# Optimization experiments

Hardware: AMD Instinct MI355X
Metric: run time of the kernel (lower is better)

The kernel has to match this reference:

```python
import jax, jax.numpy as jnp
import numpy as np
import math

D_MODEL = 512
N_HEADS = 8
D_K = 64
BS = 16
SEQ = 512


def setup_inputs() -> dict:
    key = jax.random.key(0)
    ks = jax.random.split(key, 15)
    f = lambda k, sh, s=1.0: jax.random.normal(k, sh, dtype=jnp.float32) * s
    inp = {}
    for i, n in enumerate(["q_mean", "q_cov", "k_mean", "k_cov", "v_mean", "v_cov"]):
        inp[n] = f(ks[i], (BS, SEQ, D_MODEL))
    wscale = 1.0 / math.sqrt(D_MODEL)  # ~xavier
    for i, n in enumerate(["Wq_mean", "Wq_cov", "Wk_mean", "Wk_cov", "Wv_mean", "Wv_cov", "Wo_mean", "Wo_cov"]):
        inp[n] = f(ks[6 + i], (D_MODEL, D_MODEL), wscale)
    inp["gammas"] = f(ks[14], (N_HEADS, 1, 1), 0.5)  # xavier on (h,1,1)
    # causal mask: attend to positions j <= i
    inp["mask"] = jnp.tril(jnp.ones((SEQ, SEQ), dtype=jnp.int32))[None, None]
    return inp


def _heads(x, W):
    # torch Linear: x @ W.T ; bias is 0 by init. -> [bs, h, S, d_k]
    bs = x.shape[0]
    return (x @ W.T).reshape(bs, -1, N_HEADS, D_K).transpose(0, 2, 1, 3)


def _uattention(qm, qc, km, kc, vm, vc, mask, gammas):
    # Wasserstein-2 distance between diagonal Gaussians, fused into matmuls
    mean_d = (-2.0 * jnp.einsum('bhsd,bhtd->bhst', qm, km)
              + jnp.sum(qm ** 2, -1, keepdims=True)
              + jnp.sum(km ** 2, -1, keepdims=True).swapaxes(-1, -2))
    sqc = jnp.sqrt(jnp.clip(qc, 1e-24))
    skc = jnp.sqrt(jnp.clip(kc, 1e-24))
    cov_d = (-2.0 * jnp.einsum('bhsd,bhtd->bhst', sqc, skc)
             + jnp.sum(qc, -1, keepdims=True)
             + jnp.sum(kc, -1, keepdims=True).swapaxes(-1, -2))
    scores = -(mean_d + cov_d) / math.sqrt(D_K)  # [bs,h,S,S]

    maskb = (mask == 0)
    maskf = mask.astype(scores.dtype)

    def _dist(s):
        s_ = jax.nn.softmax(jnp.where(maskb, -1e32, s), axis=-1) * maskf
        cum = jnp.cumsum(s_, axis=-1)
        tot = jnp.sum(s_, axis=-1, keepdims=True)
        idx = jnp.arange(SEQ)
        pos = jnp.abs(idx[None, :] - idx[:, None]).astype(jnp.float32)[None, None]
        return jnp.sqrt(jnp.clip((tot - cum) * pos, 0.0))

    dist_scores = jax.lax.stop_gradient(_dist(scores))  # torch: no_grad + detach
    gamma = -jax.nn.softplus(gammas)[None]  # [1,h,1,1]
    total_effect = jnp.clip(jnp.exp(dist_scores * gamma), 1e-5, 1e5)
    scores = jnp.where(maskb, -1e32, scores * total_effect)
    scores = jax.nn.softmax(scores, axis=-1)
    scores = scores.at[:, :, 0, :].set(0.0)  # zero_pad
    out_mean = jnp.einsum('bhst,bhtd->bhsd', scores, vm)
    out_cov = jnp.einsum('bhst,bhtd->bhsd', scores ** 2, vc)
    return out_mean, out_cov


def reference(q_mean, q_cov, k_mean, k_cov, v_mean, v_cov,
              Wq_mean, Wq_cov, Wk_mean, Wk_cov, Wv_mean, Wv_cov,
              Wo_mean, Wo_cov, gammas, mask):
    bs = q_mean.shape[0]
    qm = _heads(q_mean, Wq_mean)
    qc = _heads(q_cov, Wq_cov)
    km = _heads(k_mean, Wk_mean)
    kc = _heads(k_cov, Wk_cov)
    vm = _heads(v_mean, Wv_mean)
    vc = _heads(v_cov, Wv_cov)
    om, oc = _uattention(qm, qc, km, kc, vm, vc, mask, gammas)
    cm = om.transpose(0, 2, 1, 3).reshape(bs, -1, D_MODEL)
    cc = oc.transpose(0, 2, 1, 3).reshape(bs, -1, D_MODEL)
    return cm @ Wo_mean.T, cc @ Wo_cov.T
```

## Files before the change

### kernel.cpp

```cpp
#include <hip/hip_runtime.h>
#include <hip/hip_bf16.h>

#define SEQ    512
#define DMODEL 512
#define NHEAD  8
#define DK     64
#define BS     16
#define NBH    (BS*NHEAD)
#define HSZ    (SEQ*DK)
#define L2E    1.4426950408889634f

typedef __attribute__((ext_vector_type(8))) short bf16x8;
typedef __attribute__((ext_vector_type(4))) float f32x4;

#define MFMA32(A,B,C) __builtin_amdgcn_mfma_f32_16x16x32_bf16(A,B,C,0,0,0)

#define WS_GAM 16ull
#define WS_AQM 256ull
#define WS_AQC (WS_AQM +  65536ull)
#define WS_BKM (WS_AQM + 131072ull)
#define WS_BKC (WS_AQM + 196608ull)
#define WS_AQF (WS_AQM + 262144ull)
#define WS_BKF (WS_AQM + 327680ull)
#define WS_OM  1048576ull
#define WS_OC  (WS_OM + 4194304ull)
#define WS_BF  (WS_OC + 4194304ull)
#define ARRE   4194304ull
#define A_QMH 0
#define A_QML 1
#define A_SCH 2
#define A_SCL 3
#define A_KMH 4
#define A_SKH 6
#define A_VMT 8
#define A_VCT 9

__device__ __forceinline__ unsigned short* warr(float* wsf, int idx) {
  return (unsigned short*)(wsf + WS_BF) + (size_t)idx * ARRE;
}

__device__ __forceinline__ float bf2f(unsigned short h) {
  union { float f; unsigned u; } v; v.u = ((unsigned)h) << 16; return v.f;
}
__device__ __forceinline__ unsigned short f2bf(float f) {
  union { float f; unsigned u; } v; v.f = f;
  unsigned u = v.u;
  u += 0x7FFFu + ((u >> 16) & 1u);
  return (unsigned short)(u >> 16);
}
__device__ __forceinline__ void ld8_f32(const float* p, float* v) {
  float4 a = *(const float4*)p; float4 b = *(const float4*)(p+4);
  v[0]=a.x;v[1]=a.y;v[2]=a.z;v[3]=a.w;v[4]=b.x;v[5]=b.y;v[6]=b.z;v[7]=b.w;
}
__device__ __forceinline__ unsigned pk2bf(float a, float b) {
  union { float f; unsigned u; } x, y;
  x.f = a; y.f = b;
  return __builtin_amdgcn_perm(y.u + 0x8000u, x.u + 0x8000u, 0x07060302u);
}
__device__ __forceinline__ uint4 cvt8r(const float* t8) {
  uint4 h;
  h.x = pk2bf(t8[0], t8[1]);
  h.y = pk2bf(t8[2], t8[3]);
  h.z = pk2bf(t8[4], t8[5]);
  h.w = pk2bf(t8[6], t8[7]);
  return h;
}
__device__ __forceinline__ uint4 cvt8h(const float* p) {
  float t8[8]; ld8_f32(p, t8); return cvt8r(t8);
}

__global__ void k_gamma(const float* __restrict__ g_in, float* __restrict__ wsf) {
  int t = threadIdx.x;
  if (t >= NHEAD) return;
  float g = g_in[t];
  float sp = (g > 20.f) ? g : log1pf(expf(g));
  float gl = sp * L2E;
  (wsf + WS_GAM)[t] = gl * gl;
}

__global__ __launch_bounds__(256) void k_projM(
    const float* xqm, const float* xqc, const float* xkm, const float* xkc,
    const float* xvm, const float* xvc,
    const float* wqm, const float* wqc, const float* wkm, const float* wkc,
    const float* wvm, const float* wvc,
    float* wsf)
{
  __shared__ __align__(16) unsigned short Ah[4096];
  __shared__ __align__(16) unsigned short Bh[4096];
  const int y = blockIdx.y;
  const float* X; const float* W;
  unsigned short *outh = nullptr, *outl = nullptr;
  float* sums = nullptr;
  float qscale = 1.0f; int mode = 0;
  switch (y) {
    case 0: X=xqm; W=wqm; outh=warr(wsf,A_QMH); outl=warr(wsf,A_QML); sums=wsf+WS_AQM; qscale=0.25f*L2E; mode=0; break;
    case 1: X=xkm; W=wkm; outh=warr(wsf,A_KMH); outl=nullptr;         sums=wsf+WS_BKM; qscale=1.0f;      mode=0; break;
    case 2: X=xqc; W=wqc; outh=warr(wsf,A_SCH); outl=warr(wsf,A_SCL); sums=wsf+WS_AQC; qscale=0.25f*L2E; mode=1; break;
    case 3: X=xkc; W=wkc; outh=warr(wsf,A_SKH); outl=nullptr;         sums=wsf+WS_BKC; qscale=1.0f;      mode=1; break;
    case 4: X=xvm; W=wvm; outh=warr(wsf,A_VMT); mode=2; break;
    default:X=xvc; W=wvc; outh=warr(wsf,A_VCT); mode=2; break;
  }
  const int tid = threadIdx.x;
  const int l = tid & 63, li = l & 15, lg = l >> 4;
  const int w = tid >> 6, wr = w >> 1, wc = w & 1;
  const int blk = blockIdx.x;
  const int xcd = blk & 7, qq = blk >> 3;
  const int m0 = (xcd*8 + (qq & 7)) * 128;
  const int n0 = (qq >> 3) * 128;
  const int r0 = tid >> 2, c0 = tid & 3, r1 = r0 + 64;
  const int wo0 = r0*64 + ((c0 ^ ((r0>>1)&3))*16);
  const int wo1 = r1*64 + ((c0 ^ ((r1>>1)&3))*16);
  int roA[4], roB[4];
#pragma unroll
  for (int mi = 0; mi < 4; ++mi) {
    int r  = wr*64 + mi*16 + li;
    roA[mi] = r*64 + ((lg ^ ((r>>1)&3))*16);
    int rn = wc*64 + mi*16 + li;
    roB[mi] = rn*64 + ((lg ^ ((rn>>1)&3))*16);
  }
  const float* xp0 = X + (size_t)(m0+r0)*DMODEL + c0*8;
  const float* xp1 = X + (size_t)(m0+r1)*DMODEL + c0*8;
  const float* wp0 = W + (size_t)(n0+r0)*DMODEL + c0*8;
  const float* wp1 = W + (size_t)(n0+r1)*DMODEL + c0*8;
  uint4 a0 = cvt8h(xp0);
  uint4 a1 = cvt8h(xp1);
  uint4 b0 = cvt8h(wp0);
  uint4 b1 = cvt8h(wp1);

  f32x4 acc[4][4];
  f32x4 z = {0.f,0.f,0.f,0.f};
#pragma unroll
  for (int a = 0; a < 4; ++a)
#pragma unroll
    for (int b = 0; b < 4; ++b) acc[a][b] = z;

  for (int kt = 0; kt < DMODEL; kt += 32) {
    __syncthreads();
    *(uint4*)((char*)Ah + wo0) = a0;
    *(uint4*)((char*)Ah + wo1) = a1;
    *(uint4*)((char*)Bh + wo0) = b0;
    *(uint4*)((char*)Bh + wo1) = b1;
    __syncthreads();
    if (kt + 32 < DMODEL) {
      a0 = cvt8h(xp0 + kt + 32);
      a1 = cvt8h(xp1 + kt + 32);
      b0 = cvt8h(wp0 + kt + 32);
      b1 = cvt8h(wp1 + kt + 32);
    }
    bf16x8 ah[4], bh[4];
#pragma unroll
    for (int mi = 0; mi < 4; ++mi) {
      ah[mi] = *(const bf16x8*)((const char*)Ah + roA[mi]);
      bh[mi] = *(const bf16x8*)((const char*)Bh + roB[mi]);
    }
#pragma unroll
    for (int mi = 0; mi < 4; ++mi)
#pragma unroll
      for (int nj = 0; nj < 4; ++nj)
        acc[mi][nj] = MFMA32(ah[mi], bh[nj], acc[mi][nj]);
  }

  const int head = ((n0 >> 6) + wc);
  if (mode <= 1) {
    const bool kside = (outl == nullptr);
#pragma unroll
    for (int mi = 0; mi < 4; ++mi)
#pragma unroll
      for (int reg = 0; reg < 4; ++reg) {
        float rs = 0.f;
#pragma unroll
        for (int nj = 0; nj < 4; ++nj) {
          float v = acc[mi][nj][reg];
          if (mode == 0) {
            float vs = (kside) ? bf2f(f2bf(v)) : v;
            rs += vs*vs;
          } else {
            rs += v;
          }
        }
        rs += __shfl_xor(rs, 1); rs += __shfl_xor(rs, 2);
        rs += __shfl_xor(rs, 4); rs += __shfl_xor(rs, 8);
        if (li == 0) {
          int m = m0 + wr*64 + mi*16 + 4*lg + reg;
          sums[((size_t)(m >> 9)*NHEAD + head)*SEQ + (m & 511)] = rs;
        }
      }
#pragma unroll
    for (int mi = 0; mi < 4; ++mi)
#pragma unroll
      for (int nj = 0; nj < 4; ++nj)
#pragma unroll
        for (int reg = 0; reg < 4; ++reg) {
          float v = acc[mi][nj][reg];
          if (mode == 1) v = sqrtf(fmaxf(v, 1e-24f));
          v *= qscale;
          unsigned short h16 = f2bf(v);
          int m = m0 + wr*64 + mi*16 + 4*lg + reg;
          int n = n0 + wc*64 + nj*16 + li;
          size_t dst = ((size_t)((m >> 9)*NHEAD + (n >> 6))*SEQ + (m & 511))*DK + (n & 63);
          outh[dst] = h16;
          if (outl) outl[dst] = f2bf(v - bf2f(h16));
        }
  } else {
#pragma unroll
    for (int mi = 0; mi < 4; ++mi)
#pragma unroll
      for (int nj = 0; nj < 4; ++nj) {
        int mb = m0 + wr*64 + mi*16 + 4*lg;
        int n = n0 + wc*64 + nj*16 + li;
        int b = mb >> 9, s = mb & 511, d = n & 63;
        unsigned e0 = f2bf(acc[mi][nj][0]);
        unsigned e1 = f2bf(acc[mi][nj][1]);
        unsigned e2 = f2bf(acc[mi][nj][2]);
        unsigned e3 = f2bf(acc[mi][nj][3]);
        uint2 pk; pk.x = e0 | (e1 << 16); pk.y = e2 | (e3 << 16);
        *(uint2*)(outh + ((size_t)(b*NHEAD + head)*DK + d)*SEQ + s) = pk;
      }
  }
}

__global__ void k_sumAB(float* wsf) {
  int i = blockIdx.x * 256 + threadIdx.x;
  if (i < NBH*SEQ) {
    (wsf+WS_AQF)[i] = (0.125f*L2E) * ((wsf+WS_AQM)[i] + (wsf+WS_AQC)[i]);
    (wsf+WS_BKF)[i] = (0.125f*L2E) * ((wsf+WS_BKM)[i] + (wsf+WS_BKC)[i]);
  }
}

__global__ __launch_bounds__(128) void k_attn2(float* wsf)
{
  __shared__ float s_bk[SEQ];
  __shared__ float s_tot[2][16];
  __shared__ __align__(16) float s_acc[64][33];

  const unsigned short* qmh = warr(wsf, A_QMH);
  const unsigned short* qml = warr(wsf, A_QML);
  const unsigned short* sch = warr(wsf, A_SCH);
  const unsigned short* scl = warr(wsf, A_SCL);
  const unsigned short* kmh = warr(wsf, A_KMH);
  const unsigned short* skh = warr(wsf, A_SKH);
  const unsigned short* vmT = warr(wsf, A_VMT);
  const unsigned short* vcT = warr(wsf, A_VCT);
  float* omF = wsf + WS_OM;
  float* ocF = wsf + WS_OC;
  const float* AqF = wsf + WS_AQF;
  const float* BkF = wsf + WS_BKF;

  const int tid = threadIdx.x;
  const int l = tid & 63, li = l & 15, lg = l >> 4;
  const int w = tid >> 6;
  const int blk = blockIdx.x;
  const int xcd = blk & 7;
  const int q   = blk >> 3;
  const int bh  = xcd*16 + (q & 15);
  const int rt  = 31 - (q >> 4);
  const int i = rt*16 + li;
  const int ntile = rt + 1;
  const int h0 = (ntile + 1) >> 1;
  const int tstart = w ? h0 : 0;
  const int tend   = w ? ntile : h0;
  const float gam2 = (wsf + WS_GAM)[bh & (NHEAD-1)];
  const float aq = AqF[(size_t)bh*SEQ + i];

  for (int idx = tid; idx < SEQ; idx += 128) s_bk[idx] = BkF[(size_t)bh*SEQ + idx];

  bf16x8 qf[8];
  {
    const unsigned short* qb[4] = {qmh, qml, sch, scl};
#pragma unroll
    for (int part = 0; part < 2; ++part)
#pragma unroll
      for (int hl = 0; hl < 2; ++hl)
#pragma unroll
        for (int ks = 0; ks < 2; ++ks)
          qf[part*4 + ks*2 + hl] =
            *(const bf16x8*)(qb[part*2+hl] + ((size_t)bh*SEQ + i)*DK + ks*32 + lg*8);
  }
  __syncthreads();

  auto score_tile = [&](int t, float* s) {
    const int j0 = t*16;
    f32x4 accA = {0.f,0.f,0.f,0.f};
    f32x4 accB = {0.f,0.f,0.f,0.f};
    const size_t krow = ((size_t)bh*SEQ + j0 + li)*DK + lg*8;
#pragma unroll
    for (int part = 0; part < 2; ++part) {
      const unsigned short* khp = part ? skh : kmh;
#pragma unroll
      for (int ks = 0; ks < 2; ++ks) {
        bf16x8 kh = *(const bf16x8*)(khp + krow + ks*32);
        accA = MFMA32(kh, qf[part*4+ks*2+0], accA);
        accB = MFMA32(kh, qf[part*4+ks*2+1], accB);
      }
    }
    const float4 bk4 = *(const float4*)&s_bk[j0 + lg*4];
    float bks[4] = {bk4.x, bk4.y, bk4.z, bk4.w};
#pragma unroll
    for (int r = 0; r < 4; ++r) {
      int j = j0 + lg*4 + r;
      float v = (accA[r] + accB[r]) - aq - bks[r];
      s[r] = (j > i) ? -3.0e38f : v;
    }
  };

  float totl = 0.f;
  for (int t = tstart; t < tend; ++t) {
    float s[4]; score_tile(t, s);
    totl += exp2f(s[0]) + exp2f(s[1]) + exp2f(s[2]) + exp2f(s[3]);
  }
  totl += __shfl_xor(totl, 16); totl += __shfl_xor(totl, 32);
  if (lg == 0) s_tot[w][li] = totl;
  __syncthreads();
  const float tot = fmaxf(s_tot[0][li] + s_tot[1][li], 1e-35f);
  float run = w ? s_tot[0][li] : 0.f;
  const float g2i = gam2 / tot;

  f32x4 accm[4], accc[4];
  {
    f32x4 z = {0.f,0.f,0.f,0.f};
#pragma unroll
    for (int dt = 0; dt < 4; ++dt) { accm[dt] = z; accc[dt] = z; }
  }
  float sum2l = 0.f;

  auto scan_tile = [&](int t, float* p) {
    float s[4]; score_tile(t, s);
    float e0 = exp2f(s[0]), e1 = exp2f(s[1]), e2 = exp2f(s[2]), e3 = exp2f(s[3]);
    float c0 = e0, c1 = c0+e1, c2 = c1+e2, c3 = c2+e3;
    float a = __shfl_up(c3, 16), b = __shfl_up(c3, 32), c = __shfl_up(c3, 48);
    float excl = (lg >= 1 ? a : 0.f) + (lg >= 2 ? b : 0.f) + (lg >= 3 ? c : 0.f);
    float base = run + excl;
    run = __shfl(base + c3, li + 48);
    float posb = (float)(i - t*16 - lg*4);
    float cums[4] = {base+c0, base+c1, base+c2, base+c3};
#pragma unroll
    for (int r = 0; r < 4; ++r) {
      float t4 = fmaxf((tot - cums[r]) * (posb - (float)r) * g2i, 0.f);
      float d = sqrtf(t4);
      float eff = fmaxf(exp2f(-d), 1e-5f);
      p[r] = exp2f(s[r] * eff);
      sum2l += p[r];
    }
  };

  for (int t0 = tstart; t0 < tend; t0 += 2) {
    const bool hasB = (t0 + 1) < tend;
    const int j0A = t0*16;
    const int j0B = hasB ? j0A + 16 : j0A;
    union V16 { struct { uint2 lo, hi; } u; bf16x8 v; };
    V16 vm_[4], vc_[4];
#pragma unroll
    for (int dt = 0; dt < 4; ++dt) {
      const size_t vrow = ((size_t)bh*DK + dt*16 + li)*SEQ;
      vm_[dt].u.lo = *(const uint2*)(vmT + vrow + j0A + lg*4);
      vm_[dt].u.hi = *(const uint2*)(vmT + vrow + j0B + lg*4);
      vc_[dt].u.lo = *(const uint2*)(vcT + vrow + j0A + lg*4);
      vc_[dt].u.hi = *(const uint2*)(vcT + vrow + j0B + lg*4);
    }
    float pA[4], pB[4];
    scan_tile(t0, pA);
    if (hasB) scan_tile(t0+1, pB);
    else { pB[0]=pB[1]=pB[2]=pB[3] = 0.f; }
    union PU { uint4 u; bf16x8 v; } pm, pc;
    pm.u.x = pk2bf(pA[0], pA[1]); pm.u.y = pk2bf(pA[2], pA[3]);
    pm.u.z = pk2bf(pB[0], pB[1]); pm.u.w = pk2bf(pB[2], pB[3]);
    pc.u.x = pk2bf(pA[0]*pA[0], pA[1]*pA[1]); pc.u.y = pk2bf(pA[2]*pA[2], pA[3]*pA[3]);
    pc.u.z = pk2bf(pB[0]*pB[0], pB[1]*pB[1]); pc.u.w = pk2bf(pB[2]*pB[2], pB[3]*pB[3]);
#pragma unroll
    for (int dt = 0; dt < 4; ++dt) {
      accm[dt] = MFMA32(vm_[dt].v, pm.v, accm[dt]);
      accc[dt] = MFMA32(vc_[dt].v, pc.v, accc[dt]);
    }
  }

  sum2l += __shfl_xor(sum2l, 16); sum2l += __shfl_xor(sum2l, 32);
  __syncthreads();
  if (w == 1) {
#pragma unroll
    for (int dt = 0; dt < 4; ++dt)
#pragma unroll
      for (int reg = 0; reg < 4; ++reg) {
        s_acc[l][dt*4 + reg]      = accm[dt][reg];
        s_acc[l][16 + dt*4 + reg] = accc[dt][reg];
      }
    if (lg == 0) s_tot[1][li] = sum2l;
  }
  __syncthreads();
  if (w == 0) {
    const float sum2g = sum2l + s_tot[1][li];
    const float inv2 = 1.0f / sum2g;
    const float inv2c = inv2 * inv2;
    const bool zero = (i == 0);
    float* om_p = omF + ((size_t)bh*SEQ + i)*DK;
    float* oc_p = ocF + ((size_t)bh*SEQ + i)*DK;
#pragma unroll
    for (int dt = 0; dt < 4; ++dt) {
      float4 vm4, vc4;
      vm4.x = (accm[dt][0] + s_acc[l][dt*4+0]) * inv2;
      vm4.y = (accm[dt][1] + s_acc[l][dt*4+1]) * inv2;
      vm4.z = (accm[dt][2] + s_acc[l][dt*4+2]) * inv2;
      vm4.w = (accm[dt][3] + s_acc[l][dt*4+3]) * inv2;
      vc4.x = (accc[dt][0] + s_acc[l][16+dt*4+0]) * inv2c;
      vc4.y = (accc[dt][1] + s_acc[l][16+dt*4+1]) * inv2c;
      vc4.z = (accc[dt][2] + s_acc[l][16+dt*4+2]) * inv2c;
      vc4.w = (accc[dt][3] + s_acc[l][16+dt*4+3]) * inv2c;
      if (zero) { vm4 = make_float4(0.f,0.f,0.f,0.f); vc4 = vm4; }
      *(float4*)(om_p + dt*16 + lg*4) = vm4;
      *(float4*)(oc_p + dt*16 + lg*4) = vc4;
    }
  }
}

__global__ __launch_bounds__(256) void k_outM(float* wsf,
                                              const float* w_mean, const float* w_cov,
                                              float* outp)
{
  __shared__ __align__(16) unsigned short Ah[4096];
  __shared__ __align__(16) unsigned short Bh[4096];
  const int y = blockIdx.y;
  const float* A = wsf + (y ? WS_OC : WS_OM);
  const float* W = y ? w_cov : w_mean;
  float* out = outp + (size_t)y * 4194304ull;

  const int tid = threadIdx.x;
  const int l = tid & 63, li = l & 15, lg = l >> 4;
  const int w = tid >> 6, wr = w >> 1, wc = w & 1;
  const int blk = blockIdx.x;
  const int xcd = blk & 7, qq = blk >> 3;
  const int m0 = (xcd*8 + (qq & 7)) * 128;
  const int n0 = (qq >> 3) * 128;
  const int r0 = tid >> 2, c0 = tid & 3, r1 = r0 + 64;
  const int wo0 = r0*64 + ((c0 ^ ((r0>>1)&3))*16);
  const int wo1 = r1*64 + ((c0 ^ ((r1>>1)&3))*16);
  int roA[4], roB[4];
#pragma unroll
  for (int mi = 0; mi < 4; ++mi) {
    int r  = wr*64 + mi*16 + li;
    roA[mi] = r*64 + ((lg ^ ((r>>1)&3))*16);
    int rn = wc*64 + mi*16 + li;
    roB[mi] = rn*64 + ((lg ^ ((rn>>1)&3))*16);
  }
  const int mA0 = m0 + r0, mA1 = m0 + r1;
  const size_t abase0 = ((size_t)(mA0 >> 9) * NHEAD * SEQ + (mA0 & 511)) * DK;
  const size_t abase1 = ((size_t)(mA1 >> 9) * NHEAD * SEQ + (mA1 & 511)) * DK;
  const float* wp0 = W + (size_t)(n0 + r0)*DMODEL + c0*8;
  const float* wp1 = W + (size_t)(n0 + r1)*DMODEL + c0*8;

  auto acvt = [&](size_t abase, int k) -> uint4 {
    const float* p = A + abase + (size_t)(k >> 6) * (SEQ*DK) + (k & 63);
    return cvt8h(p);
  };

  int k0 = c0*8;
  uint4 a0 = acvt(abase0, k0);
  uint4 a1 = acvt(abase1, k0);
  uint4 b0 = cvt8h(wp0);
  uint4 b1 = cvt8h(wp1);

  f32x4 acc[4][4];
  f32x4 z = {0.f,0.f,0.f,0.f};
#pragma unroll
  for (int a = 0; a < 4; ++a)
#pragma unroll
    for (int b = 0; b < 4; ++b) acc[a][b] = z;

  for (int kt = 0; kt < DMODEL; kt += 32) {
    __syncthreads();
    *(uint4*)((char*)Ah + wo0) = a0;
    *(uint4*)((char*)Ah + wo1) = a1;
    *(uint4*)((char*)Bh + wo0) = b0;
    *(uint4*)((char*)Bh + wo1) = b1;
    __syncthreads();
    if (kt + 32 < DMODEL) {
      int kn = kt + 32 + c0*8;
      a0 = acvt(abase0, kn);
      a1 = acvt(abase1, kn);
      b0 = cvt8h(wp0 + kt + 32);
      b1 = cvt8h(wp1 + kt + 32);
    }
    bf16x8 ah[4], bh[4];
#pragma unroll
    for (int mi = 0; mi < 4; ++mi) {
      ah[mi] = *(const bf16x8*)((const char*)Ah + roA[mi]);
      bh[mi] = *(const bf16x8*)((const char*)Bh + roB[mi]);
    }
#pragma unroll
    for (int mi = 0; mi < 4; ++mi)
#pragma unroll
      for (int nj = 0; nj < 4; ++nj)
        acc[mi][nj] = MFMA32(ah[mi], bh[nj], acc[mi][nj]);
  }
#pragma unroll
  for (int mi = 0; mi < 4; ++mi)
#pragma unroll
    for (int nj = 0; nj < 4; ++nj)
#pragma unroll
      for (int reg = 0; reg < 4; ++reg) {
        int m = m0 + wr*64 + mi*16 + 4*lg + reg;
        int n = n0 + wc*64 + nj*16 + li;
        out[(size_t)m*DMODEL + n] = acc[mi][nj][reg];
      }
}

extern "C" void kernel_launch(void* const* d_in, const int* in_sizes, int n_in,
                              void* d_out, int out_size, void* d_ws, size_t ws_size,
                              hipStream_t stream) {
  (void)in_sizes; (void)n_in; (void)out_size; (void)ws_size;
  float* wsf = (float*)d_ws;

  k_gamma<<<1, 64, 0, stream>>>((const float*)d_in[14], wsf);
  k_projM<<<dim3(256, 6), 256, 0, stream>>>(
      (const float*)d_in[0], (const float*)d_in[1],
      (const float*)d_in[2], (const float*)d_in[3],
      (const float*)d_in[4], (const float*)d_in[5],
      (const float*)d_in[6], (const float*)d_in[7],
      (const float*)d_in[8], (const float*)d_in[9],
      (const float*)d_in[10], (const float*)d_in[11],
      wsf);
  k_sumAB<<<256, 256, 0, stream>>>(wsf);
  k_attn2<<<4096, 128, 0, stream>>>(wsf);
  k_outM<<<dim3(256, 2), 256, 0, stream>>>(wsf, (const float*)d_in[12],
                                           (const float*)d_in[13], (float*)d_out);
}
```

Measured before the change: 241.0 us.

## Cache attention scores in LDS and pair causal row tiles per block

The attention kernel now writes the first-pass scores into a swizzled shared-memory buffer, so the second pass reads them back instead of recomputing the QK MFMAs and reloading K. Each block handles two row tiles (rt and 31-rt) so every block does the same amount of causal work, and the grid is halved. K fragments for the next tile are prefetched during the score loop. In exchange, each block uses about 35KB of LDS, which can lower occupancy, and each block runs longer.

```diff
diff --git a/kernel.cpp b/kernel.cpp
--- a/kernel.cpp
+++ b/kernel.cpp
@@ -229,9 +229,10 @@
 
 __global__ __launch_bounds__(128) void k_attn2(float* wsf)
 {
+  __shared__ __align__(16) float s_s[16*544];
   __shared__ float s_bk[SEQ];
   __shared__ float s_tot[2][16];
-  __shared__ __align__(16) float s_acc[64][33];
+  float (*s_acc)[33] = (float(*)[33])s_s;
 
   const unsigned short* qmh = warr(wsf, A_QMH);
   const unsigned short* qml = warr(wsf, A_QML);
@@ -253,160 +254,181 @@
   const int xcd = blk & 7;
   const int q   = blk >> 3;
   const int bh  = xcd*16 + (q & 15);
-  const int rt  = 31 - (q >> 4);
-  const int i = rt*16 + li;
-  const int ntile = rt + 1;
-  const int h0 = (ntile + 1) >> 1;
-  const int tstart = w ? h0 : 0;
-  const int tend   = w ? ntile : h0;
+  const int pp  = q >> 4;
   const float gam2 = (wsf + WS_GAM)[bh & (NHEAD-1)];
-  const float aq = AqF[(size_t)bh*SEQ + i];
 
   for (int idx = tid; idx < SEQ; idx += 128) s_bk[idx] = BkF[(size_t)bh*SEQ + idx];
 
-  bf16x8 qf[8];
-  {
-    const unsigned short* qb[4] = {qmh, qml, sch, scl};
-#pragma unroll
-    for (int part = 0; part < 2; ++part)
-#pragma unroll
-      for (int hl = 0; hl < 2; ++hl)
-#pragma unroll
-        for (int ks = 0; ks < 2; ++ks)
-          qf[part*4 + ks*2 + hl] =
-            *(const bf16x8*)(qb[part*2+hl] + ((size_t)bh*SEQ + i)*DK + ks*32 + lg*8);
-  }
-  __syncthreads();
-
-  auto score_tile = [&](int t, float* s) {
-    const int j0 = t*16;
-    f32x4 accA = {0.f,0.f,0.f,0.f};
-    f32x4 accB = {0.f,0.f,0.f,0.f};
-    const size_t krow = ((size_t)bh*SEQ + j0 + li)*DK + lg*8;
-#pragma unroll
-    for (int part = 0; part < 2; ++part) {
-      const unsigned short* khp = part ? skh : kmh;
-#pragma unroll
-      for (int ks = 0; ks < 2; ++ks) {
-        bf16x8 kh = *(const bf16x8*)(khp + krow + ks*32);
-        accA = MFMA32(kh, qf[part*4+ks*2+0], accA);
-        accB = MFMA32(kh, qf[part*4+ks*2+1], accB);
-      }
-    }
-    const float4 bk4 = *(const float4*)&s_bk[j0 + lg*4];
-    float bks[4] = {bk4.x, bk4.y, bk4.z, bk4.w};
-#pragma unroll
-    for (int r = 0; r < 4; ++r) {
-      int j = j0 + lg*4 + r;
-      float v = (accA[r] + accB[r]) - aq - bks[r];
-      s[r] = (j > i) ? -3.0e38f : v;
-    }
+  auto sidx = [&](int t) -> int {
+    int c = t*16 + lg*4;
+    return li*544 + (c ^ ((li & 7) << 2));
   };
 
-  float totl = 0.f;
-  for (int t = tstart; t < tend; ++t) {
-    float s[4]; score_tile(t, s);
-    totl += exp2f(s[0]) + exp2f(s[1]) + exp2f(s[2]) + exp2f(s[3]);
-  }
-  totl += __shfl_xor(totl, 16); totl += __shfl_xor(totl, 32);
-  if (lg == 0) s_tot[w][li] = totl;
-  __syncthreads();
-  const float tot = fmaxf(s_tot[0][li] + s_tot[1][li], 1e-35f);
-  float run = w ? s_tot[0][li] : 0.f;
-  const float g2i = gam2 / tot;
-
-  f32x4 accm[4], accc[4];
-  {
-    f32x4 z = {0.f,0.f,0.f,0.f};
-#pragma unroll
-    for (int dt = 0; dt < 4; ++dt) { accm[dt] = z; accc[dt] = z; }
-  }
-  float sum2l = 0.f;
-
-  auto scan_tile = [&](int t, float* p) {
-    float s[4]; score_tile(t, s);
-    float e0 = exp2f(s[0]), e1 = exp2f(s[1]), e2 = exp2f(s[2]), e3 = exp2f(s[3]);
-    float c0 = e0, c1 = c0+e1, c2 = c1+e2, c3 = c2+e3;
-    float a = __shfl_up(c3, 16), b = __shfl_up(c3, 32), c = __shfl_up(c3, 48);
-    float excl = (lg >= 1 ? a : 0.f) + (lg >= 2 ? b : 0.f) + (lg >= 3 ? c : 0.f);
-    float base = run + excl;
-    run = __shfl(base + c3, li + 48);
-    float posb = (float)(i - t*16 - lg*4);
-    float cums[4] = {base+c0, base+c1, base+c2, base+c3};
-#pragma unroll
-    for (int r = 0; r < 4; ++r) {
-      float t4 = fmaxf((tot - cums[r]) * (posb - (float)r) * g2i, 0.f);
-      float d = sqrtf(t4);
-      float eff = fmaxf(exp2f(-d), 1e-5f);
-      p[r] = exp2f(s[r] * eff);
-      sum2l += p[r];
-    }
-  };
-
-  for (int t0 = tstart; t0 < tend; t0 += 2) {
-    const bool hasB = (t0 + 1) < tend;
-    const int j0A = t0*16;
-    const int j0B = hasB ? j0A + 16 : j0A;
-    union V16 { struct { uint2 lo, hi; } u; bf16x8 v; };
-    V16 vm_[4], vc_[4];
-#pragma unroll
-    for (int dt = 0; dt < 4; ++dt) {
-      const size_t vrow = ((size_t)bh*DK + dt*16 + li)*SEQ;
-      vm_[dt].u.lo = *(const uint2*)(vmT + vrow + j0A + lg*4);
-      vm_[dt].u.hi = *(const uint2*)(vmT + vrow + j0B + lg*4);
-      vc_[dt].u.lo = *(const uint2*)(vcT + vrow + j0A + lg*4);
-      vc_[dt].u.hi = *(const uint2*)(vcT + vrow + j0B + lg*4);
-    }
-    float pA[4], pB[4];
-    scan_tile(t0, pA);
-    if (hasB) scan_tile(t0+1, pB);
-    else { pB[0]=pB[1]=pB[2]=pB[3] = 0.f; }
-    union PU { uint4 u; bf16x8 v; } pm, pc;
-    pm.u.x = pk2bf(pA[0], pA[1]); pm.u.y = pk2bf(pA[2], pA[3]);
-    pm.u.z = pk2bf(pB[0], pB[1]); pm.u.w = pk2bf(pB[2], pB[3]);
-    pc.u.x = pk2bf(pA[0]*pA[0], pA[1]*pA[1]); pc.u.y = pk2bf(pA[2]*pA[2], pA[3]*pA[3]);
-    pc.u.z = pk2bf(pB[0]*pB[0], pB[1]*pB[1]); pc.u.w = pk2bf(pB[2]*pB[2], pB[3]*pB[3]);
-#pragma unroll
-    for (int dt = 0; dt < 4; ++dt) {
-      accm[dt] = MFMA32(vm_[dt].v, pm.v, accm[dt]);
-      accc[dt] = MFMA32(vc_[dt].v, pc.v, accc[dt]);
-    }
-  }
-
-  sum2l += __shfl_xor(sum2l, 16); sum2l += __shfl_xor(sum2l, 32);
-  __syncthreads();
-  if (w == 1) {
-#pragma unroll
-    for (int dt = 0; dt < 4; ++dt)
-#pragma unroll
-      for (int reg = 0; reg < 4; ++reg) {
-        s_acc[l][dt*4 + reg]      = accm[dt][reg];
-        s_acc[l][16 + dt*4 + reg] = accc[dt][reg];
-      }
-    if (lg == 0) s_tot[1][li] = sum2l;
-  }
-  __syncthreads();
-  if (w == 0) {
-    const float sum2g = sum2l + s_tot[1][li];
-    const float inv2 = 1.0f / sum2g;
-    const float inv2c = inv2 * inv2;
-    const bool zero = (i == 0);
-    float* om_p = omF + ((size_t)bh*SEQ + i)*DK;
-    float* oc_p = ocF + ((size_t)bh*SEQ + i)*DK;
-#pragma unroll
-    for (int dt = 0; dt < 4; ++dt) {
-      float4 vm4, vc4;
-      vm4.x = (accm[dt][0] + s_acc[l][dt*4+0]) * inv2;
-      vm4.y = (accm[dt][1] + s_acc[l][dt*4+1]) * inv2;
-      vm4.z = (accm[dt][2] + s_acc[l][dt*4+2]) * inv2;
-      vm4.w = (accm[dt][3] + s_acc[l][dt*4+3]) * inv2;
-      vc4.x = (accc[dt][0] + s_acc[l][16+dt*4+0]) * inv2c;
-      vc4.y = (accc[dt][1] + s_acc[l][16+dt*4+1]) * inv2c;
-      vc4.z = (accc[dt][2] + s_acc[l][16+dt*4+2]) * inv2c;
-      vc4.w = (accc[dt][3] + s_acc[l][16+dt*4+3]) * inv2c;
-      if (zero) { vm4 = make_float4(0.f,0.f,0.f,0.f); vc4 = vm4; }
-      *(float4*)(om_p + dt*16 + lg*4) = vm4;
-      *(float4*)(oc_p + dt*16 + lg*4) = vc4;
+  for (int ph = 0; ph < 2; ++ph) {
+    const int rt = ph ? pp : (31 - pp);
+    const int i = rt*16 + li;
+    const int ntile = rt + 1;
+    const int h0 = (ntile + 1) >> 1;
+    const int tstart = w ? h0 : 0;
+    const int tend   = w ? ntile : h0;
+    const float aq = AqF[(size_t)bh*SEQ + i];
+
+    __syncthreads();
+
+    bf16x8 qf[8];
+    {
+      const unsigned short* qb[4] = {qmh, qml, sch, scl};
+#pragma unroll
+      for (int part = 0; part < 2; ++part)
+#pragma unroll
+        for (int hl = 0; hl < 2; ++hl)
+#pragma unroll
+          for (int ks = 0; ks < 2; ++ks)
+            qf[part*4 + ks*2 + hl] =
+              *(const bf16x8*)(qb[part*2+hl] + ((size_t)bh*SEQ + i)*DK + ks*32 + lg*8);
+    }
+
+    auto kload = [&](int t, bf16x8* kr) {
+      const size_t kr0 = ((size_t)bh*SEQ + t*16 + li)*DK + lg*8;
+      kr[0] = *(const bf16x8*)(kmh + kr0);
+      kr[1] = *(const bf16x8*)(kmh + kr0 + 32);
+      kr[2] = *(const bf16x8*)(skh + kr0);
+      kr[3] = *(const bf16x8*)(skh + kr0 + 32);
+    };
+
+    float totl = 0.f;
+    {
+      bf16x8 kc[4], kn[4];
+      if (tstart < tend) kload(tstart, kc);
+      for (int t = tstart; t < tend; ++t) {
+        const bool more = (t + 1) < tend;
+        if (more) kload(t + 1, kn);
+        f32x4 accA = {0.f,0.f,0.f,0.f};
+        f32x4 accB = {0.f,0.f,0.f,0.f};
+        accA = MFMA32(kc[0], qf[0], accA); accB = MFMA32(kc[0], qf[1], accB);
+        accA = MFMA32(kc[1], qf[2], accA); accB = MFMA32(kc[1], qf[3], accB);
+        accA = MFMA32(kc[2], qf[4], accA); accB = MFMA32(kc[2], qf[5], accB);
+        accA = MFMA32(kc[3], qf[6], accA); accB = MFMA32(kc[3], qf[7], accB);
+        const float4 bk4 = *(const float4*)&s_bk[t*16 + lg*4];
+        float s0 = (accA[0]+accB[0]) - aq - bk4.x;
+        float s1 = (accA[1]+accB[1]) - aq - bk4.y;
+        float s2 = (accA[2]+accB[2]) - aq - bk4.z;
+        float s3 = (accA[3]+accB[3]) - aq - bk4.w;
+        const int jb = t*16 + lg*4;
+        if (jb + 0 > i) s0 = -3.0e38f;
+        if (jb + 1 > i) s1 = -3.0e38f;
+        if (jb + 2 > i) s2 = -3.0e38f;
+        if (jb + 3 > i) s3 = -3.0e38f;
+        totl += exp2f(s0) + exp2f(s1) + exp2f(s2) + exp2f(s3);
+        *(float4*)&s_s[sidx(t)] = make_float4(s0, s1, s2, s3);
+        if (more) {
+#pragma unroll
+          for (int x = 0; x < 4; ++x) kc[x] = kn[x];
+        }
+      }
+    }
+    totl += __shfl_xor(totl, 16); totl += __shfl_xor(totl, 32);
+    if (lg == 0) s_tot[w][li] = totl;
+    __syncthreads();
+    const float tot = fmaxf(s_tot[0][li] + s_tot[1][li], 1e-35f);
+    float run = w ? s_tot[0][li] : 0.f;
+    const float g2i = gam2 / tot;
+
+    f32x4 accm[4], accc[4];
+    {
+      f32x4 z = {0.f,0.f,0.f,0.f};
+#pragma unroll
+      for (int dt = 0; dt < 4; ++dt) { accm[dt] = z; accc[dt] = z; }
+    }
+    float sum2l = 0.f;
+
+    auto scan_tile = [&](int t, float* p) {
+      const float4 sv = *(const float4*)&s_s[sidx(t)];
+      const float e0 = exp2f(sv.x), e1 = exp2f(sv.y),
+                  e2 = exp2f(sv.z), e3 = exp2f(sv.w);
+      float c0 = e0, c1 = c0+e1, c2 = c1+e2, c3 = c2+e3;
+      float a = __shfl_up(c3, 16), b = __shfl_up(c3, 32), c = __shfl_up(c3, 48);
+      float excl = (lg >= 1 ? a : 0.f) + (lg >= 2 ? b : 0.f) + (lg >= 3 ? c : 0.f);
+      float base = run + excl;
+      run = __shfl(base + c3, li + 48);
+      float posb = (float)(i - t*16 - lg*4);
+      float cums[4] = {base+c0, base+c1, base+c2, base+c3};
+      float ss[4] = {sv.x, sv.y, sv.z, sv.w};
+#pragma unroll
+      for (int r = 0; r < 4; ++r) {
+        float t4 = fmaxf((tot - cums[r]) * (posb - (float)r) * g2i, 0.f);
+        float d = sqrtf(t4);
+        float eff = fmaxf(exp2f(-d), 1e-5f);
+        p[r] = exp2f(ss[r] * eff);
+        sum2l += p[r];
+      }
+    };
+
+    for (int t0 = tstart; t0 < tend; t0 += 2) {
+      const bool hasB = (t0 + 1) < tend;
+      const int j0A = t0*16;
+      const int j0B = hasB ? j0A + 16 : j0A;
+      union V16 { struct { uint2 lo, hi; } u; bf16x8 v; };
+      V16 vm_[4], vc_[4];
+#pragma unroll
+      for (int dt = 0; dt < 4; ++dt) {
+        const size_t vrow = ((size_t)bh*DK + dt*16 + li)*SEQ;
+        vm_[dt].u.lo = *(const uint2*)(vmT + vrow + j0A + lg*4);
+        vm_[dt].u.hi = *(const uint2*)(vmT + vrow + j0B + lg*4);
+        vc_[dt].u.lo = *(const uint2*)(vcT + vrow + j0A + lg*4);
+        vc_[dt].u.hi = *(const uint2*)(vcT + vrow + j0B + lg*4);
+      }
+      float pA[4], pB[4];
+      scan_tile(t0, pA);
+      if (hasB) scan_tile(t0+1, pB);
+      else { pB[0]=pB[1]=pB[2]=pB[3] = 0.f; }
+      union PU { uint4 u; bf16x8 v; } pm, pc;
+      pm.u.x = pk2bf(pA[0], pA[1]); pm.u.y = pk2bf(pA[2], pA[3]);
+      pm.u.z = pk2bf(pB[0], pB[1]); pm.u.w = pk2bf(pB[2], pB[3]);
+      pc.u.x = pk2bf(pA[0]*pA[0], pA[1]*pA[1]); pc.u.y = pk2bf(pA[2]*pA[2], pA[3]*pA[3]);
+      pc.u.z = pk2bf(pB[0]*pB[0], pB[1]*pB[1]); pc.u.w = pk2bf(pB[2]*pB[2], pB[3]*pB[3]);
+#pragma unroll
+      for (int dt = 0; dt < 4; ++dt) {
+        accm[dt] = MFMA32(vm_[dt].v, pm.v, accm[dt]);
+        accc[dt] = MFMA32(vc_[dt].v, pc.v, accc[dt]);
+      }
+    }
+
+    sum2l += __shfl_xor(sum2l, 16); sum2l += __shfl_xor(sum2l, 32);
+    __syncthreads();
+    if (w == 1) {
+#pragma unroll
+      for (int dt = 0; dt < 4; ++dt)
+#pragma unroll
+        for (int reg = 0; reg < 4; ++reg) {
+          s_acc[l][dt*4 + reg]      = accm[dt][reg];
+          s_acc[l][16 + dt*4 + reg] = accc[dt][reg];
+        }
+      if (lg == 0) s_tot[1][li] = sum2l;
+    }
+    __syncthreads();
+    if (w == 0) {
+      const float sum2g = sum2l + s_tot[1][li];
+      const float inv2 = 1.0f / sum2g;
+      const float inv2c = inv2 * inv2;
+      const bool zero = (i == 0);
+      float* om_p = omF + ((size_t)bh*SEQ + i)*DK;
+      float* oc_p = ocF + ((size_t)bh*SEQ + i)*DK;
+#pragma unroll
+      for (int dt = 0; dt < 4; ++dt) {
+        float4 vm4, vc4;
+        vm4.x = (accm[dt][0] + s_acc[l][dt*4+0]) * inv2;
+        vm4.y = (accm[dt][1] + s_acc[l][dt*4+1]) * inv2;
+        vm4.z = (accm[dt][2] + s_acc[l][dt*4+2]) * inv2;
+        vm4.w = (accm[dt][3] + s_acc[l][dt*4+3]) * inv2;
+        vc4.x = (accc[dt][0] + s_acc[l][16+dt*4+0]) * inv2c;
+        vc4.y = (accc[dt][1] + s_acc[l][16+dt*4+1]) * inv2c;
+        vc4.z = (accc[dt][2] + s_acc[l][16+dt*4+2]) * inv2c;
+        vc4.w = (accc[dt][3] + s_acc[l][16+dt*4+3]) * inv2c;
+        if (zero) { vm4 = make_float4(0.f,0.f,0.f,0.f); vc4 = vm4; }
+        *(float4*)(om_p + dt*16 + lg*4) = vm4;
+        *(float4*)(oc_p + dt*16 + lg*4) = vc4;
+      }
     }
   }
 }
@@ -518,7 +540,7 @@
       (const float*)d_in[10], (const float*)d_in[11],
       wsf);
   k_sumAB<<<256, 256, 0, stream>>>(wsf);
-  k_attn2<<<4096, 128, 0, stream>>>(wsf);
+  k_attn2<<<2048, 128, 0, stream>>>(wsf);
   k_outM<<<dim3(256, 2), 256, 0, stream>>>(wsf, (const float*)d_in[12],
                                            (const float*)d_in[13], (float*)d_out);
 }
```

After: 217.3 us. -9.8%, faster.
